# Performance work log

Hardware: AMD Instinct MI355X
Metric: run time of the kernel (lower is better)

Reference implementation:

```python
import jax, jax.numpy as jnp
import numpy as np

T, B, H, V = 512, 256, 256, 32000

def setup_inputs() -> dict:
    key = jax.random.key(0)
    ks = jax.random.split(key, 8)
    s = 1.0 / np.sqrt(H)  # PyTorch LSTMCell init scale
    return {
        "enc_inputs": jax.random.randint(ks[0], (T, B), 0, V),
        "h0": jnp.zeros((B, H), jnp.float32),
        "c0": jnp.zeros((B, H), jnp.float32),
        "embed": jax.random.normal(ks[1], (V, H), jnp.float32),
        "W_ih": jax.random.uniform(ks[2], (4 * H, H), jnp.float32, -s, s),
        "W_hh": jax.random.uniform(ks[3], (4 * H, H), jnp.float32, -s, s),
        "b_ih": jax.random.uniform(ks[4], (4 * H,), jnp.float32, -s, s),
        "b_hh": jax.random.uniform(ks[5], (4 * H,), jnp.float32, -s, s),
    }

def _lstm_cell(x, h, c, W_ih, W_hh, b_ih, b_hh):
    # gates: [B, 4H], PyTorch gate order i, f, g, o
    gates = x @ W_ih.T + b_ih + h @ W_hh.T + b_hh
    i, f, g, o = jnp.split(gates, 4, axis=-1)
    i = jax.nn.sigmoid(i)
    f = jax.nn.sigmoid(f)
    g = jnp.tanh(g)
    o = jax.nn.sigmoid(o)
    c_new = f * c + i * g
    h_new = o * jnp.tanh(c_new)
    return h_new, c_new

def reference(enc_inputs, h0, c0, embed, W_ih, W_hh, b_ih, b_hh):
    # enc_inputs: [T, B] int; embeddings: [T, B, H]
    emb = embed[enc_inputs]

    def step(carry, x_t):
        h, c = carry
        h, c = _lstm_cell(x_t, h, c, W_ih, W_hh, b_ih, b_hh)
        return (h, c), None

    (h, c), _ = jax.lax.scan(step, (h0, c0), emb)
    return (h, c)
```

## Files before the change

kernel.cpp:

```cpp
#include <hip/hip_runtime.h>
#include <hip/hip_bf16.h>
#include <stddef.h>
#include <stdint.h>

#define T_STEPS 512
#define B_SZ 256
#define H_SZ 256
#define G4H 1024
#define PH 264
#define HS_PAR (16 * PH)

#define LOG2E 1.4426950408889634f
#define TWO_LOG2E 2.8853900817779268f

typedef __attribute__((ext_vector_type(8))) short bf16x8;
typedef __attribute__((ext_vector_type(4))) float f32x4;

__device__ __forceinline__ unsigned short f2bf(float f) {
  union { float f; unsigned u; } v; v.f = f;
  unsigned r = v.u + 0x7fffu + ((v.u >> 16) & 1u);
  return (unsigned short)(r >> 16);
}
__device__ __forceinline__ float bf2f(unsigned short h) {
  union { unsigned u; float f; } v; v.u = ((unsigned)h) << 16; return v.f;
}
__device__ __forceinline__ float exp2_hw(float x) { return __builtin_amdgcn_exp2f(x); }
__device__ __forceinline__ float rcp_hw(float x) { return __builtin_amdgcn_rcpf(x); }

__global__ void prep_kernel(const float* __restrict__ h0, const float* __restrict__ c0,
                            const float* __restrict__ W_ih, const float* __restrict__ W_hh,
                            const float* __restrict__ b_ih, const float* __restrict__ b_hh,
                            unsigned short* __restrict__ Wih_bf, unsigned short* __restrict__ Whh_bf,
                            float* __restrict__ bias, unsigned short* __restrict__ h_st,
                            float* __restrict__ c_st) {
  int i = blockIdx.x * 256 + threadIdx.x;
  int stride = gridDim.x * 256;
  for (int k = i; k < G4H * H_SZ; k += stride) {
    int gate = k >> 16;
    float sc = (gate == 2) ? TWO_LOG2E : LOG2E;
    Wih_bf[k] = f2bf(W_ih[k] * sc);
    Whh_bf[k] = f2bf(W_hh[k] * sc);
  }
  for (int k = i; k < B_SZ * H_SZ; k += stride) {
    h_st[k] = f2bf(h0[k]);
    c_st[k] = c0[k];
  }
  for (int k = i; k < G4H; k += stride) {
    float sc = ((k >> 8) == 2) ? TWO_LOG2E : LOG2E;
    bias[k] = (b_ih[k] + b_hh[k]) * sc;
  }
}

__global__ __launch_bounds__(256, 2) void xgate_kernel(
    const int* __restrict__ enc, const float* __restrict__ embed,
    const unsigned short* __restrict__ Wih_bf, const float* __restrict__ bias,
    unsigned short* __restrict__ xg, int t0, int Ci) {
  __shared__ __align__(16) unsigned short As[64][264];
  const int tid = threadIdx.x;
  const int mbase = blockIdx.x * 64;

  {
    int r = tid >> 2, q = tid & 3;
    int mg = mbase + r;
    int s = mg >> 8, b = mg & 255;
    int vid = enc[(t0 + s) * B_SZ + b];
    const float4* src = (const float4*)(embed + (size_t)vid * H_SZ) + q * 16;
#pragma unroll
    for (int j = 0; j < 16; ++j) {
      float4 x = src[j];
      ushort4 o;
      o.x = f2bf(x.x); o.y = f2bf(x.y); o.z = f2bf(x.z); o.w = f2bf(x.w);
      *(ushort4*)&As[r][q * 64 + j * 4] = o;
    }
  }
  __syncthreads();

  const int wave = tid >> 6, lane = tid & 63;
  const int lrow = lane & 15, quad = lane >> 4;

  bf16x8 af[4][8];
#pragma unroll
  for (int mt = 0; mt < 4; ++mt)
#pragma unroll
    for (int ks = 0; ks < 8; ++ks)
      af[mt][ks] = *(const bf16x8*)&As[mt * 16 + lrow][ks * 32 + quad * 8];

  const int t_loc = mbase >> 8;

  for (int g = 0; g < 4; ++g) {
#pragma unroll
    for (int nt = 0; nt < 4; ++nt) {
      const int j = wave * 64 + nt * 16 + lrow;
      const int nrow = g * 256 + j;
      const unsigned short* wrow = Wih_bf + (size_t)nrow * H_SZ + quad * 8;
      bf16x8 bf[8];
#pragma unroll
      for (int ks = 0; ks < 8; ++ks) bf[ks] = *(const bf16x8*)(wrow + ks * 32);
      const float bs = bias[nrow];
#pragma unroll
      for (int mt = 0; mt < 4; ++mt) {
        f32x4 a = {0.f, 0.f, 0.f, 0.f};
#pragma unroll
        for (int ks = 0; ks < 8; ++ks)
          a = __builtin_amdgcn_mfma_f32_16x16x32_bf16(af[mt][ks], bf[ks], a, 0, 0, 0);
        const int bg = ((mbase >> 4) & 15) + mt;
        const int tid2 = (wave * 4 + nt) * 64 + quad * 16 + lrow;
        const size_t off = (((size_t)t_loc * 16 + bg) * 1024 + tid2) * 16 + g * 4;
        ushort4 o;
        o.x = f2bf(a[0] + bs); o.y = f2bf(a[1] + bs);
        o.z = f2bf(a[2] + bs); o.w = f2bf(a[3] + bs);
        *(ushort4*)(xg + off) = o;
      }
    }
  }
}

__global__ __launch_bounds__(1024) void lstm_kernel(
    const unsigned short* __restrict__ Whh_bf, const unsigned short* __restrict__ xg,
    unsigned short* __restrict__ h_st, float* __restrict__ c_st,
    float* __restrict__ out, int t0, int Ci) {
  __shared__ __align__(16) unsigned short Hs[2 * HS_PAR];
  __shared__ __align__(16) unsigned short Wg[16 * 4096];

  const int tid = threadIdx.x, w = tid >> 6, lane = tid & 63;
  const int lrow = lane & 15, quad = lane >> 4;
  const int b0 = blockIdx.x * 16;
  const int jcol = w * 16 + lrow;

  bf16x8 wf0[8], wf1[8];
  {
    const unsigned short* wr0 = Whh_bf + (size_t)(0 * 256 + jcol) * H_SZ + quad * 8;
    const unsigned short* wr1 = Whh_bf + (size_t)(1 * 256 + jcol) * H_SZ + quad * 8;
#pragma unroll
    for (int ks = 0; ks < 8; ++ks) {
      wf0[ks] = *(const bf16x8*)(wr0 + ks * 32);
      wf1[ks] = *(const bf16x8*)(wr1 + ks * 32);
    }
  }
  {
    const unsigned short* wr2 = Whh_bf + (size_t)(2 * 256 + jcol) * H_SZ + quad * 8;
#pragma unroll
    for (int ks = 0; ks < 8; ++ks) {
      bf16x8 v = *(const bf16x8*)(wr2 + ks * 32);
      *(bf16x8*)&Wg[w * 4096 + ks * 512 + lane * 8] = v;
    }
  }
  const unsigned short* wr3 = Whh_bf + (size_t)(3 * 256 + jcol) * H_SZ + quad * 8;

  if (tid < 256) {
    int row = tid >> 4, c16 = (tid & 15) * 16;
    const unsigned short* src = h_st + (size_t)(b0 + row) * H_SZ + c16;
    *(uint4*)&Hs[row * PH + c16] = *(const uint4*)src;
    *(uint4*)&Hs[row * PH + c16 + 8] = *(const uint4*)(src + 8);
  }

  float creg[4], hv[4];
#pragma unroll
  for (int r = 0; r < 4; ++r)
    creg[r] = c_st[(size_t)(b0 + quad * 4 + r) * H_SZ + jcol];

  const unsigned short* pxg = xg + ((size_t)blockIdx.x * 1024 + tid) * 16;
  uint4 xa0 = *(const uint4*)pxg;
  uint4 xa1 = *(const uint4*)(pxg + 8);
  __syncthreads();

  const int af_base = lrow * (PH * 2) + quad * 16;
  const int hw_base = (quad * 4) * (PH * 2) + jcol * 2;
  const int PAR_B = HS_PAR * 2;
  const unsigned short* wlds = &Wg[w * 4096 + lane * 8];

#pragma unroll 1
  for (int s = 0; s < Ci; ++s) {
    const int rp = (s & 1) * PAR_B;
    const int wp = PAR_B - rp;
    const char* hsr = (const char*)Hs + af_base + rp;
    char* hsw = (char*)Hs + hw_base + wp;

    f32x4 a0 = {0.f, 0.f, 0.f, 0.f}, a2 = a0;
#pragma unroll
    for (int ks = 0; ks < 8; ++ks) {
      bf16x8 af = *(const bf16x8*)(hsr + ks * 64);
      bf16x8 w2 = *(const bf16x8*)(wlds + ks * 512);
      a0 = __builtin_amdgcn_mfma_f32_16x16x32_bf16(af, wf0[ks], a0, 0, 0, 0);
      a2 = __builtin_amdgcn_mfma_f32_16x16x32_bf16(af, w2, a2, 0, 0, 0);
    }

    pxg += (size_t)((s + 1 < Ci) ? 16 * 1024 * 16 : 0);
    uint4 xb0 = *(const uint4*)pxg;
    uint4 xb1 = *(const uint4*)(pxg + 8);

    const unsigned short* xv0 = (const unsigned short*)&xa0;
    const unsigned short* xv1 = (const unsigned short*)&xa1;
    float ig[4];
#pragma unroll
    for (int r = 0; r < 4; ++r) {
      float zi = a0[r] + bf2f(xv0[r]);
      float zg = a2[r] + bf2f(xv1[r]);
      float ei = exp2_hw(-zi);
      float eg = exp2_hw(zg);
      ig[r] = (eg - 1.0f) * rcp_hw((1.0f + ei) * (eg + 1.0f));
    }

    f32x4 a1 = {0.f, 0.f, 0.f, 0.f}, a3 = a1;
#pragma unroll
    for (int ks = 0; ks < 8; ++ks) {
      bf16x8 af = *(const bf16x8*)(hsr + ks * 64);
      bf16x8 w3 = *(const bf16x8*)(wr3 + ks * 32);
      a1 = __builtin_amdgcn_mfma_f32_16x16x32_bf16(af, wf1[ks], a1, 0, 0, 0);
      a3 = __builtin_amdgcn_mfma_f32_16x16x32_bf16(af, w3, a3, 0, 0, 0);
    }

#pragma unroll
    for (int r = 0; r < 4; ++r) {
      float zf = a1[r] + bf2f(xv0[4 + r]);
      float zo = a3[r] + bf2f(xv1[4 + r]);
      float ef = exp2_hw(-zf);
      float c = fmaf(creg[r], rcp_hw(1.0f + ef), ig[r]);
      creg[r] = c;
      float eo = exp2_hw(-zo);
      float ec = exp2_hw(fminf(c * TWO_LOG2E, 126.0f));
      float h = (ec - 1.0f) * rcp_hw((1.0f + eo) * (ec + 1.0f));
      hv[r] = h;
      *(unsigned short*)(hsw + r * (PH * 2)) = f2bf(h);
    }
    xa0 = xb0;
    xa1 = xb1;
    __syncthreads();
  }

#pragma unroll
  for (int r = 0; r < 4; ++r) {
    const size_t gidx = (size_t)(b0 + quad * 4 + r) * H_SZ + jcol;
    h_st[gidx] = f2bf(hv[r]);
    c_st[gidx] = creg[r];
  }
  if (t0 + Ci == T_STEPS) {
#pragma unroll
    for (int r = 0; r < 4; ++r) {
      const size_t gidx = (size_t)(b0 + quad * 4 + r) * H_SZ + jcol;
      out[gidx] = hv[r];
      out[(size_t)B_SZ * H_SZ + gidx] = creg[r];
    }
  }
}

extern "C" void kernel_launch(void* const* d_in, const int* in_sizes, int n_in,
                              void* d_out, int out_size, void* d_ws, size_t ws_size,
                              hipStream_t stream) {
  const int* enc = (const int*)d_in[0];
  const float* h0 = (const float*)d_in[1];
  const float* c0 = (const float*)d_in[2];
  const float* embed = (const float*)d_in[3];
  const float* W_ih = (const float*)d_in[4];
  const float* W_hh = (const float*)d_in[5];
  const float* b_ih = (const float*)d_in[6];
  const float* b_hh = (const float*)d_in[7];
  float* out = (float*)d_out;

  char* ws = (char*)d_ws;
  unsigned short* Wih_bf = (unsigned short*)(ws);
  unsigned short* Whh_bf = (unsigned short*)(ws + (512 << 10));
  float* bias = (float*)(ws + (1024 << 10));
  unsigned short* h_st = (unsigned short*)(ws + (1028 << 10));
  float* c_st = (float*)(ws + (1156 << 10));
  const size_t fixed = (size_t)(1412) << 10;
  unsigned short* xg = (unsigned short*)(ws + fixed);

  const size_t per_step = (size_t)B_SZ * G4H * 2;
  int C = 1;
  if (ws_size > fixed + per_step) {
    size_t c = (ws_size - fixed) / per_step;
    C = (c > T_STEPS) ? T_STEPS : (int)c;
  }

  prep_kernel<<<dim3(256), dim3(256), 0, stream>>>(h0, c0, W_ih, W_hh, b_ih, b_hh,
                                                   Wih_bf, Whh_bf, bias, h_st, c_st);
  for (int t0 = 0; t0 < T_STEPS; t0 += C) {
    int Ci = (T_STEPS - t0 < C) ? (T_STEPS - t0) : C;
    xgate_kernel<<<dim3(Ci * 4), dim3(256), 0, stream>>>(enc, embed, Wih_bf, bias,
                                                         xg, t0, Ci);
    lstm_kernel<<<dim3(16), dim3(1024), 0, stream>>>(Whh_bf, xg, h_st, c_st,
                                                     out, t0, Ci);
  }
}
```

Measured before the change: 2.013 ms.

## Keep output-gate recurrent weights in registers and unroll the timestep loop by two

The output-gate W_hh fragment was previously re-read from global memory on every timestep. It is now preloaded once into registers, alongside the input and forget gate fragments. The MFMA accumulators are seeded with the precomputed input projection, which removes the separate adds. The step loop is unrolled by two with ping-pong registers for the xg prefetch, and the sync is replaced by an explicit lgkmcnt wait, s_barrier and sched_barrier. Holding 24 weight fragments per lane raises VGPR pressure under launch_bounds(1024) and risks spills.

```diff
diff --git a/kernel.cpp b/kernel.cpp
--- a/kernel.cpp
+++ b/kernel.cpp
@@ -26,6 +26,25 @@
 }
 __device__ __forceinline__ float exp2_hw(float x) { return __builtin_amdgcn_exp2f(x); }
 __device__ __forceinline__ float rcp_hw(float x) { return __builtin_amdgcn_rcpf(x); }
+
+__device__ __forceinline__ f32x4 exp2_4(f32x4 x) {
+  f32x4 r;
+  r[0] = exp2_hw(x[0]); r[1] = exp2_hw(x[1]);
+  r[2] = exp2_hw(x[2]); r[3] = exp2_hw(x[3]);
+  return r;
+}
+__device__ __forceinline__ f32x4 rcp_4(f32x4 x) {
+  f32x4 r;
+  r[0] = rcp_hw(x[0]); r[1] = rcp_hw(x[1]);
+  r[2] = rcp_hw(x[2]); r[3] = rcp_hw(x[3]);
+  return r;
+}
+__device__ __forceinline__ f32x4 min_4(f32x4 x, float c) {
+  f32x4 r;
+  r[0] = fminf(x[0], c); r[1] = fminf(x[1], c);
+  r[2] = fminf(x[2], c); r[3] = fminf(x[3], c);
+  return r;
+}
 
 __global__ void prep_kernel(const float* __restrict__ h0, const float* __restrict__ c0,
                             const float* __restrict__ W_ih, const float* __restrict__ W_hh,
@@ -127,14 +146,16 @@
   const int b0 = blockIdx.x * 16;
   const int jcol = w * 16 + lrow;
 
-  bf16x8 wf0[8], wf1[8];
+  bf16x8 wf0[8], wf1[8], wf3[8];
   {
     const unsigned short* wr0 = Whh_bf + (size_t)(0 * 256 + jcol) * H_SZ + quad * 8;
     const unsigned short* wr1 = Whh_bf + (size_t)(1 * 256 + jcol) * H_SZ + quad * 8;
+    const unsigned short* wr3 = Whh_bf + (size_t)(3 * 256 + jcol) * H_SZ + quad * 8;
 #pragma unroll
     for (int ks = 0; ks < 8; ++ks) {
       wf0[ks] = *(const bf16x8*)(wr0 + ks * 32);
       wf1[ks] = *(const bf16x8*)(wr1 + ks * 32);
+      wf3[ks] = *(const bf16x8*)(wr3 + ks * 32);
     }
   }
   {
@@ -145,7 +166,6 @@
       *(bf16x8*)&Wg[w * 4096 + ks * 512 + lane * 8] = v;
     }
   }
-  const unsigned short* wr3 = Whh_bf + (size_t)(3 * 256 + jcol) * H_SZ + quad * 8;
 
   if (tid < 256) {
     int row = tid >> 4, c16 = (tid & 15) * 16;
@@ -154,14 +174,16 @@
     *(uint4*)&Hs[row * PH + c16 + 8] = *(const uint4*)(src + 8);
   }
 
-  float creg[4], hv[4];
+  f32x4 creg4, hv4;
 #pragma unroll
   for (int r = 0; r < 4; ++r)
-    creg[r] = c_st[(size_t)(b0 + quad * 4 + r) * H_SZ + jcol];
-
+    creg4[r] = c_st[(size_t)(b0 + quad * 4 + r) * H_SZ + jcol];
+
+  const size_t XG_STRIDE = (size_t)16 * 1024 * 16;
   const unsigned short* pxg = xg + ((size_t)blockIdx.x * 1024 + tid) * 16;
   uint4 xa0 = *(const uint4*)pxg;
   uint4 xa1 = *(const uint4*)(pxg + 8);
+  uint4 xb0, xb1;
   __syncthreads();
 
   const int af_base = lrow * (PH * 2) + quad * 16;
@@ -169,77 +191,78 @@
   const int PAR_B = HS_PAR * 2;
   const unsigned short* wlds = &Wg[w * 4096 + lane * 8];
 
+#define LSTM_STEP(XA0, XA1, XB0, XB1, RP, PREF)                                   \
+  do {                                                                            \
+    const char* hsr = (const char*)Hs + af_base + (RP);                           \
+    char* hsw = (char*)Hs + hw_base + (PAR_B - (RP));                             \
+    if (PREF) pxg += XG_STRIDE;                                                   \
+    XB0 = *(const uint4*)pxg;                                                     \
+    XB1 = *(const uint4*)(pxg + 8);                                               \
+    const unsigned short* xv0 = (const unsigned short*)&XA0;                      \
+    const unsigned short* xv1 = (const unsigned short*)&XA1;                      \
+                        \
+    f32x4 a0 = {bf2f(xv0[0]), bf2f(xv0[1]), bf2f(xv0[2]), bf2f(xv0[3])};          \
+    f32x4 a2 = {bf2f(xv1[0]), bf2f(xv1[1]), bf2f(xv1[2]), bf2f(xv1[3])};          \
+    _Pragma("unroll")                                                             \
+    for (int ks = 0; ks < 8; ++ks) {                                              \
+      bf16x8 af = *(const bf16x8*)(hsr + ks * 64);                                \
+      bf16x8 w2 = *(const bf16x8*)(wlds + ks * 512);                              \
+      a0 = __builtin_amdgcn_mfma_f32_16x16x32_bf16(af, wf0[ks], a0, 0, 0, 0);     \
+      a2 = __builtin_amdgcn_mfma_f32_16x16x32_bf16(af, w2, a2, 0, 0, 0);          \
+    }                                                                             \
+                               \
+    f32x4 ei = exp2_4(-a0);                                                       \
+    f32x4 eg = exp2_4(a2);                                                        \
+    f32x4 ig = (eg - 1.0f) * rcp_4((ei + 1.0f) * (eg + 1.0f));                    \
+                         \
+    f32x4 a1 = {bf2f(xv0[4]), bf2f(xv0[5]), bf2f(xv0[6]), bf2f(xv0[7])};          \
+    f32x4 a3 = {bf2f(xv1[4]), bf2f(xv1[5]), bf2f(xv1[6]), bf2f(xv1[7])};          \
+    _Pragma("unroll")                                                             \
+    for (int ks = 0; ks < 8; ++ks) {                                              \
+      bf16x8 af = *(const bf16x8*)(hsr + ks * 64);                                \
+      a1 = __builtin_amdgcn_mfma_f32_16x16x32_bf16(af, wf1[ks], a1, 0, 0, 0);     \
+      a3 = __builtin_amdgcn_mfma_f32_16x16x32_bf16(af, wf3[ks], a3, 0, 0, 0);     \
+    }                                                                             \
+                            \
+    f32x4 ef = exp2_4(-a1);                                                       \
+    f32x4 c4 = creg4 * rcp_4(ef + 1.0f) + ig;                                     \
+    creg4 = c4;                                                                   \
+    f32x4 eo = exp2_4(-a3);                                                       \
+    f32x4 ec = exp2_4(min_4(c4 * TWO_LOG2E, 126.0f));                             \
+    f32x4 h4 = (ec - 1.0f) * rcp_4((eo + 1.0f) * (ec + 1.0f));                    \
+    hv4 = h4;                                                                     \
+    *(unsigned short*)(hsw + 0 * (PH * 2)) = f2bf(h4[0]);                         \
+    *(unsigned short*)(hsw + 1 * (PH * 2)) = f2bf(h4[1]);                         \
+    *(unsigned short*)(hsw + 2 * (PH * 2)) = f2bf(h4[2]);                         \
+    *(unsigned short*)(hsw + 3 * (PH * 2)) = f2bf(h4[3]);                         \
+    asm volatile("s_waitcnt lgkmcnt(0)" ::: "memory");                            \
+    __builtin_amdgcn_s_barrier();                                                 \
+    __builtin_amdgcn_sched_barrier(0);                                            \
+  } while (0)
+
+  int s = 0;
 #pragma unroll 1
-  for (int s = 0; s < Ci; ++s) {
-    const int rp = (s & 1) * PAR_B;
-    const int wp = PAR_B - rp;
-    const char* hsr = (const char*)Hs + af_base + rp;
-    char* hsw = (char*)Hs + hw_base + wp;
-
-    f32x4 a0 = {0.f, 0.f, 0.f, 0.f}, a2 = a0;
-#pragma unroll
-    for (int ks = 0; ks < 8; ++ks) {
-      bf16x8 af = *(const bf16x8*)(hsr + ks * 64);
-      bf16x8 w2 = *(const bf16x8*)(wlds + ks * 512);
-      a0 = __builtin_amdgcn_mfma_f32_16x16x32_bf16(af, wf0[ks], a0, 0, 0, 0);
-      a2 = __builtin_amdgcn_mfma_f32_16x16x32_bf16(af, w2, a2, 0, 0, 0);
-    }
-
-    pxg += (size_t)((s + 1 < Ci) ? 16 * 1024 * 16 : 0);
-    uint4 xb0 = *(const uint4*)pxg;
-    uint4 xb1 = *(const uint4*)(pxg + 8);
-
-    const unsigned short* xv0 = (const unsigned short*)&xa0;
-    const unsigned short* xv1 = (const unsigned short*)&xa1;
-    float ig[4];
-#pragma unroll
-    for (int r = 0; r < 4; ++r) {
-      float zi = a0[r] + bf2f(xv0[r]);
-      float zg = a2[r] + bf2f(xv1[r]);
-      float ei = exp2_hw(-zi);
-      float eg = exp2_hw(zg);
-      ig[r] = (eg - 1.0f) * rcp_hw((1.0f + ei) * (eg + 1.0f));
-    }
-
-    f32x4 a1 = {0.f, 0.f, 0.f, 0.f}, a3 = a1;
-#pragma unroll
-    for (int ks = 0; ks < 8; ++ks) {
-      bf16x8 af = *(const bf16x8*)(hsr + ks * 64);
-      bf16x8 w3 = *(const bf16x8*)(wr3 + ks * 32);
-      a1 = __builtin_amdgcn_mfma_f32_16x16x32_bf16(af, wf1[ks], a1, 0, 0, 0);
-      a3 = __builtin_amdgcn_mfma_f32_16x16x32_bf16(af, w3, a3, 0, 0, 0);
-    }
-
-#pragma unroll
-    for (int r = 0; r < 4; ++r) {
-      float zf = a1[r] + bf2f(xv0[4 + r]);
-      float zo = a3[r] + bf2f(xv1[4 + r]);
-      float ef = exp2_hw(-zf);
-      float c = fmaf(creg[r], rcp_hw(1.0f + ef), ig[r]);
-      creg[r] = c;
-      float eo = exp2_hw(-zo);
-      float ec = exp2_hw(fminf(c * TWO_LOG2E, 126.0f));
-      float h = (ec - 1.0f) * rcp_hw((1.0f + eo) * (ec + 1.0f));
-      hv[r] = h;
-      *(unsigned short*)(hsw + r * (PH * 2)) = f2bf(h);
-    }
-    xa0 = xb0;
-    xa1 = xb1;
-    __syncthreads();
-  }
+  for (; s + 2 <= Ci; s += 2) {
+    LSTM_STEP(xa0, xa1, xb0, xb1, 0, true);
+    LSTM_STEP(xb0, xb1, xa0, xa1, PAR_B, s + 2 < Ci);
+  }
+  if (s < Ci) {
+    LSTM_STEP(xa0, xa1, xb0, xb1, 0, false);
+  }
+#undef LSTM_STEP
 
 #pragma unroll
   for (int r = 0; r < 4; ++r) {
     const size_t gidx = (size_t)(b0 + quad * 4 + r) * H_SZ + jcol;
-    h_st[gidx] = f2bf(hv[r]);
-    c_st[gidx] = creg[r];
+    h_st[gidx] = f2bf(hv4[r]);
+    c_st[gidx] = creg4[r];
   }
   if (t0 + Ci == T_STEPS) {
 #pragma unroll
     for (int r = 0; r < 4; ++r) {
       const size_t gidx = (size_t)(b0 + quad * 4 + r) * H_SZ + jcol;
-      out[gidx] = hv[r];
-      out[(size_t)B_SZ * H_SZ + gidx] = creg[r];
+      out[gidx] = hv4[r];
+      out[(size_t)B_SZ * H_SZ + gidx] = creg4[r];
     }
   }
 }
```

Result: slower. 2.990 ms (+48.5%).

## Fuse input-gate producers and recurrent consumers into one persistent flag-synchronized kernel

Applied to the files above, without the earlier changes.

Replaces the separate xgate and lstm kernel launches with one persistent kernel. Blocks 16 to 255 compute input-gate projections into a ring buffer in global memory, and the 16 recurrent blocks consume them chunk by chunk. Atomic producer and consumer flags with acquire/release semantics order the two sides. The goal is to overlap the input projection with the serial recurrence and to drop the launch boundaries between the phases. The risks are deadlock if all 256 blocks are not co-resident, and producer traffic competing with the latency-bound recurrent blocks.

```diff
diff --git a/kernel.cpp b/kernel.cpp
--- a/kernel.cpp
+++ b/kernel.cpp
@@ -9,6 +9,10 @@
 #define G4H 1024
 #define PH 264
 #define HS_PAR (16 * PH)
+#define NPROD 240
+#define CHUNK 16
+#define NCHUNK (T_STEPS / CHUNK)
+#define STEP_SHORTS ((size_t)16 * 1024 * 16)
 
 #define LOG2E 1.4426950408889634f
 #define TWO_LOG2E 2.8853900817779268f
@@ -26,6 +30,9 @@
 }
 __device__ __forceinline__ float exp2_hw(float x) { return __builtin_amdgcn_exp2f(x); }
 __device__ __forceinline__ float rcp_hw(float x) { return __builtin_amdgcn_rcpf(x); }
+
+__device__ int prod_flags[NCHUNK];
+__device__ int cons_flags[NCHUNK];
 
 __global__ void prep_kernel(const float* __restrict__ h0, const float* __restrict__ c0,
                             const float* __restrict__ W_ih, const float* __restrict__ W_hh,
@@ -35,6 +42,10 @@
                             float* __restrict__ c_st) {
   int i = blockIdx.x * 256 + threadIdx.x;
   int stride = gridDim.x * 256;
+  for (int k = i; k < NCHUNK; k += stride) {
+    prod_flags[k] = 0;
+    cons_flags[k] = 0;
+  }
   for (int k = i; k < G4H * H_SZ; k += stride) {
     int gate = k >> 16;
     float sc = (gate == 2) ? TWO_LOG2E : LOG2E;
@@ -241,6 +252,232 @@
       out[gidx] = hv[r];
       out[(size_t)B_SZ * H_SZ + gidx] = creg[r];
     }
+  }
+}
+
+__global__ __launch_bounds__(1024) void fused_kernel(
+    const int* __restrict__ enc, const float* __restrict__ embed,
+    const unsigned short* __restrict__ Wih_bf, const float* __restrict__ bias,
+    const unsigned short* __restrict__ Whh_bf, unsigned short* __restrict__ xg,
+    unsigned short* __restrict__ h_st, float* __restrict__ c_st,
+    float* __restrict__ out, int R) {
+  __shared__ __align__(16) unsigned char smem[147968];
+  const int blk = blockIdx.x;
+  const int tid = threadIdx.x;
+
+  if (blk >= 16) {
+    const int p = blk - 16;
+    const int t256 = tid & 255, unit = tid >> 8;
+    unsigned short* AsU = (unsigned short*)(smem + unit * 33792);
+    const int wave = t256 >> 6, lane = tid & 63;
+    const int lrow = lane & 15, quad = lane >> 4;
+
+#pragma unroll 1
+    for (int s = p; s < T_STEPS; s += NPROD) {
+      {
+        int r = t256 >> 2, q = t256 & 3;
+        int b = unit * 64 + r;
+        int vid = enc[s * B_SZ + b];
+        const float4* src = (const float4*)(embed + (size_t)vid * H_SZ) + q * 16;
+#pragma unroll
+        for (int j = 0; j < 16; ++j) {
+          float4 x = src[j];
+          ushort4 o;
+          o.x = f2bf(x.x); o.y = f2bf(x.y); o.z = f2bf(x.z); o.w = f2bf(x.w);
+          *(ushort4*)&AsU[r * 264 + q * 64 + j * 4] = o;
+        }
+      }
+      if (tid == 0) {
+        int sprev = s - R;
+        if (sprev >= 0) {
+          while (__hip_atomic_load(&cons_flags[sprev >> 4], __ATOMIC_ACQUIRE,
+                                   __HIP_MEMORY_SCOPE_AGENT) < 16)
+            __builtin_amdgcn_s_sleep(8);
+        }
+      }
+      __syncthreads();
+
+      const size_t slot = (size_t)(s % R);
+#pragma unroll 1
+      for (int mt = 0; mt < 4; ++mt) {
+        bf16x8 af[8];
+#pragma unroll
+        for (int ks = 0; ks < 8; ++ks)
+          af[ks] = *(const bf16x8*)&AsU[(mt * 16 + lrow) * 264 + ks * 32 + quad * 8];
+#pragma unroll 1
+        for (int nt = 0; nt < 4; ++nt) {
+          const int j = wave * 64 + nt * 16 + lrow;
+          f32x4 acc[4];
+          float bs[4];
+#pragma unroll
+          for (int g = 0; g < 4; ++g) {
+            const int nrow = g * 256 + j;
+            const unsigned short* wrow = Wih_bf + (size_t)nrow * H_SZ + quad * 8;
+            bf16x8 bfr[8];
+#pragma unroll
+            for (int ks = 0; ks < 8; ++ks) bfr[ks] = *(const bf16x8*)(wrow + ks * 32);
+            bs[g] = bias[nrow];
+            f32x4 a = {0.f, 0.f, 0.f, 0.f};
+#pragma unroll
+            for (int ks = 0; ks < 8; ++ks)
+              a = __builtin_amdgcn_mfma_f32_16x16x32_bf16(af[ks], bfr[ks], a, 0, 0, 0);
+            acc[g] = a;
+          }
+          const int bg = unit * 4 + mt;
+          const int tid2 = (wave * 4 + nt) * 64 + quad * 16 + lrow;
+          const size_t off = ((slot * 16 + bg) * 1024 + tid2) * 16;
+          unsigned short ov[16];
+#pragma unroll
+          for (int g = 0; g < 4; ++g)
+#pragma unroll
+            for (int r = 0; r < 4; ++r) ov[g * 4 + r] = f2bf(acc[g][r] + bs[g]);
+          *(uint4*)(xg + off) = *(const uint4*)&ov[0];
+          *(uint4*)(xg + off + 8) = *(const uint4*)&ov[8];
+        }
+      }
+      __syncthreads();
+      if (tid == 0) {
+        __threadfence();
+        __hip_atomic_fetch_add(&prod_flags[s >> 4], 1, __ATOMIC_RELEASE,
+                               __HIP_MEMORY_SCOPE_AGENT);
+      }
+    }
+    return;
+  }
+
+  unsigned short* Hs = (unsigned short*)smem;
+  unsigned short* Wg = (unsigned short*)(smem + 16896);
+
+  const int w = tid >> 6, lane = tid & 63;
+  const int lrow = lane & 15, quad = lane >> 4;
+  const int b0 = blk * 16;
+  const int jcol = w * 16 + lrow;
+
+  bf16x8 wf0[8], wf1[8];
+  {
+    const unsigned short* wr0 = Whh_bf + (size_t)(0 * 256 + jcol) * H_SZ + quad * 8;
+    const unsigned short* wr1 = Whh_bf + (size_t)(1 * 256 + jcol) * H_SZ + quad * 8;
+#pragma unroll
+    for (int ks = 0; ks < 8; ++ks) {
+      wf0[ks] = *(const bf16x8*)(wr0 + ks * 32);
+      wf1[ks] = *(const bf16x8*)(wr1 + ks * 32);
+    }
+  }
+  {
+    const unsigned short* wr2 = Whh_bf + (size_t)(2 * 256 + jcol) * H_SZ + quad * 8;
+#pragma unroll
+    for (int ks = 0; ks < 8; ++ks) {
+      bf16x8 v = *(const bf16x8*)(wr2 + ks * 32);
+      *(bf16x8*)&Wg[w * 4096 + ks * 512 + lane * 8] = v;
+    }
+  }
+  const unsigned short* wr3 = Whh_bf + (size_t)(3 * 256 + jcol) * H_SZ + quad * 8;
+
+  if (tid < 256) {
+    int row = tid >> 4, c16 = (tid & 15) * 16;
+    const unsigned short* src = h_st + (size_t)(b0 + row) * H_SZ + c16;
+    *(uint4*)&Hs[row * PH + c16] = *(const uint4*)src;
+    *(uint4*)&Hs[row * PH + c16 + 8] = *(const uint4*)(src + 8);
+  }
+
+  float creg[4], hv[4];
+#pragma unroll
+  for (int r = 0; r < 4; ++r)
+    creg[r] = c_st[(size_t)(b0 + quad * 4 + r) * H_SZ + jcol];
+
+  const unsigned short* pxg = xg;
+  uint4 xa0 = {0, 0, 0, 0}, xa1 = {0, 0, 0, 0};
+  __syncthreads();
+
+  const int af_base = lrow * (PH * 2) + quad * 16;
+  const int hw_base = (quad * 4) * (PH * 2) + jcol * 2;
+  const int PAR_B = HS_PAR * 2;
+  const unsigned short* wlds = &Wg[w * 4096 + lane * 8];
+
+#pragma unroll 1
+  for (int s = 0; s < T_STEPS; ++s) {
+    if ((s & (CHUNK - 1)) == 0) {
+      if (tid == 0) {
+        if (s > 0)
+          __hip_atomic_fetch_add(&cons_flags[(s >> 4) - 1], 1, __ATOMIC_RELEASE,
+                                 __HIP_MEMORY_SCOPE_AGENT);
+        while (__hip_atomic_load(&prod_flags[s >> 4], __ATOMIC_ACQUIRE,
+                                 __HIP_MEMORY_SCOPE_AGENT) < 16)
+          __builtin_amdgcn_s_sleep(8);
+      }
+      __syncthreads();
+      pxg = xg + (size_t)(s % R) * STEP_SHORTS + ((size_t)blk * 1024 + tid) * 16;
+      xa0 = *(const uint4*)pxg;
+      xa1 = *(const uint4*)(pxg + 8);
+    }
+
+    const int rp = (s & 1) * PAR_B;
+    const int wp = PAR_B - rp;
+    const char* hsr = (const char*)Hs + af_base + rp;
+    char* hsw = (char*)Hs + hw_base + wp;
+
+    f32x4 a0 = {0.f, 0.f, 0.f, 0.f}, a2 = a0;
+#pragma unroll
+    for (int ks = 0; ks < 8; ++ks) {
+      bf16x8 af = *(const bf16x8*)(hsr + ks * 64);
+      bf16x8 w2 = *(const bf16x8*)(wlds + ks * 512);
+      a0 = __builtin_amdgcn_mfma_f32_16x16x32_bf16(af, wf0[ks], a0, 0, 0, 0);
+      a2 = __builtin_amdgcn_mfma_f32_16x16x32_bf16(af, w2, a2, 0, 0, 0);
+    }
+
+    pxg += STEP_SHORTS;
+    uint4 xb0 = xa0, xb1 = xa1;
+    if (((s + 1) & (CHUNK - 1)) != 0) {
+      xb0 = *(const uint4*)pxg;
+      xb1 = *(const uint4*)(pxg + 8);
+    }
+
+    const unsigned short* xv0 = (const unsigned short*)&xa0;
+    const unsigned short* xv1 = (const unsigned short*)&xa1;
+    float ig[4];
+#pragma unroll
+    for (int r = 0; r < 4; ++r) {
+      float zi = a0[r] + bf2f(xv0[r]);
+      float zg = a2[r] + bf2f(xv1[r]);
+      float ei = exp2_hw(-zi);
+      float eg = exp2_hw(zg);
+      ig[r] = (eg - 1.0f) * rcp_hw((1.0f + ei) * (eg + 1.0f));
+    }
+
+    f32x4 a1 = {0.f, 0.f, 0.f, 0.f}, a3 = a1;
+#pragma unroll
+    for (int ks = 0; ks < 8; ++ks) {
+      bf16x8 af = *(const bf16x8*)(hsr + ks * 64);
+      bf16x8 w3 = *(const bf16x8*)(wr3 + ks * 32);
+      a1 = __builtin_amdgcn_mfma_f32_16x16x32_bf16(af, wf1[ks], a1, 0, 0, 0);
+      a3 = __builtin_amdgcn_mfma_f32_16x16x32_bf16(af, w3, a3, 0, 0, 0);
+    }
+
+#pragma unroll
+    for (int r = 0; r < 4; ++r) {
+      float zf = a1[r] + bf2f(xv0[4 + r]);
+      float zo = a3[r] + bf2f(xv1[4 + r]);
+      float ef = exp2_hw(-zf);
+      float c = fmaf(creg[r], rcp_hw(1.0f + ef), ig[r]);
+      creg[r] = c;
+      float eo = exp2_hw(-zo);
+      float ec = exp2_hw(fminf(c * TWO_LOG2E, 126.0f));
+      float h = (ec - 1.0f) * rcp_hw((1.0f + eo) * (ec + 1.0f));
+      hv[r] = h;
+      *(unsigned short*)(hsw + r * (PH * 2)) = f2bf(h);
+    }
+    xa0 = xb0;
+    xa1 = xb1;
+    __syncthreads();
+  }
+
+#pragma unroll
+  for (int r = 0; r < 4; ++r) {
+    const size_t gidx = (size_t)(b0 + quad * 4 + r) * H_SZ + jcol;
+    h_st[gidx] = f2bf(hv[r]);
+    c_st[gidx] = creg[r];
+    out[gidx] = hv[r];
+    out[(size_t)B_SZ * H_SZ + gidx] = creg[r];
   }
 }
 
@@ -267,19 +504,28 @@
   unsigned short* xg = (unsigned short*)(ws + fixed);
 
   const size_t per_step = (size_t)B_SZ * G4H * 2;
-  int C = 1;
+  int R = 0;
   if (ws_size > fixed + per_step) {
-    size_t c = (ws_size - fixed) / per_step;
-    C = (c > T_STEPS) ? T_STEPS : (int)c;
+    size_t r = (ws_size - fixed) / per_step;
+    R = (r > T_STEPS) ? T_STEPS : (int)r;
   }
 
   prep_kernel<<<dim3(256), dim3(256), 0, stream>>>(h0, c0, W_ih, W_hh, b_ih, b_hh,
                                                    Wih_bf, Whh_bf, bias, h_st, c_st);
-  for (int t0 = 0; t0 < T_STEPS; t0 += C) {
-    int Ci = (T_STEPS - t0 < C) ? (T_STEPS - t0) : C;
-    xgate_kernel<<<dim3(Ci * 4), dim3(256), 0, stream>>>(enc, embed, Wih_bf, bias,
-                                                         xg, t0, Ci);
-    lstm_kernel<<<dim3(16), dim3(1024), 0, stream>>>(Whh_bf, xg, h_st, c_st,
-                                                     out, t0, Ci);
-  }
-}
+
+  int Rring = R & ~(CHUNK - 1);
+  if (Rring >= 2 * CHUNK) {
+    fused_kernel<<<dim3(256), dim3(1024), 0, stream>>>(enc, embed, Wih_bf, bias,
+                                                       Whh_bf, xg, h_st, c_st, out,
+                                                       Rring);
+  } else {
+    int C = (R > 0) ? R : 1;
+    for (int t0 = 0; t0 < T_STEPS; t0 += C) {
+      int Ci = (T_STEPS - t0 < C) ? (T_STEPS - t0) : C;
+      xgate_kernel<<<dim3(Ci * 4), dim3(256), 0, stream>>>(enc, embed, Wih_bf, bias,
+                                                           xg, t0, Ci);
+      lstm_kernel<<<dim3(16), dim3(1024), 0, stream>>>(Whh_bf, xg, h_st, c_st,
+                                                       out, t0, Ci);
+    }
+  }
+}
```

Result: slower. 4.702 ms (+133.5%).
